# Kernel tuning notes

Hardware: AMD Instinct MI355X
Metric: run time of the kernel (lower is better)

## Reference

```python
import jax, jax.numpy as jnp
import numpy as np

N = 50000
E = 800000
HID = 256
HEADS1, C1 = 8, 32   # conv1: 2*out_dim=32 per head, 8 heads, concat -> 256
HEADS2, C2 = 1, 16   # conv2: out_dim=16, 1 head
NEG_SLOPE = 0.2


def setup_inputs() -> dict:
    key = jax.random.key(0)
    ks = jax.random.split(key, 12)
    x = jax.random.normal(ks[0], (N, HID), dtype=jnp.float32)
    edge_index = jax.random.randint(ks[1], (2, E), 0, N, dtype=jnp.int64)
    # GATConv #1 params (PyG: lin weight, att_src, att_dst, bias)
    W1 = jax.random.normal(ks[2], (HID, HEADS1 * C1), dtype=jnp.float32) / np.sqrt(HID)
    a1_src = jax.random.normal(ks[3], (HEADS1, C1), dtype=jnp.float32) * 0.1
    a1_dst = jax.random.normal(ks[4], (HEADS1, C1), dtype=jnp.float32) * 0.1
    b1 = jnp.zeros((HEADS1 * C1,), dtype=jnp.float32)
    # GATConv #2 params
    W2 = jax.random.normal(ks[5], (HEADS1 * C1, HEADS2 * C2), dtype=jnp.float32) / np.sqrt(HEADS1 * C1)
    a2_src = jax.random.normal(ks[6], (HEADS2, C2), dtype=jnp.float32) * 0.1
    a2_dst = jax.random.normal(ks[7], (HEADS2, C2), dtype=jnp.float32) * 0.1
    b2 = jnp.zeros((HEADS2 * C2,), dtype=jnp.float32)
    return {"x": x, "edge_index": edge_index, "W1": W1, "a1_src": a1_src,
            "a1_dst": a1_dst, "b1": b1, "W2": W2, "a2_src": a2_src,
            "a2_dst": a2_dst, "b2": b2}


def _gat_conv(x, src, dst, W, a_src, a_dst, b, heads, ch):
    n = x.shape[0]
    h = (x @ W).reshape(n, heads, ch)                      # [N,H,C]
    alpha_s = jnp.einsum('nhc,hc->nh', h, a_src)           # [N,H]
    alpha_d = jnp.einsum('nhc,hc->nh', h, a_dst)
    e = jax.nn.leaky_relu(alpha_s[src] + alpha_d[dst], NEG_SLOPE)  # [E,H]
    # segment softmax over edges grouped by destination node
    e_max = jax.ops.segment_max(e, dst, num_segments=n)
    ex = jnp.exp(e - e_max[dst])
    denom = jax.ops.segment_sum(ex, dst, num_segments=n)
    alpha = ex / denom[dst]                                # [E,H]
    msg = h[src] * alpha[..., None]                        # [E,H,C]
    out = jax.ops.segment_sum(msg, dst, num_segments=n)    # [N,H,C]
    return out.reshape(n, heads * ch) + b


def reference(x, edge_index, W1, a1_src, a1_dst, b1, W2, a2_src, a2_dst, b2):
    n = x.shape[0]
    # add self loops (PyG GATConv default) so every segment is non-empty
    loops = jnp.arange(n, dtype=edge_index.dtype)
    src = jnp.concatenate([edge_index[0], loops])
    dst = jnp.concatenate([edge_index[1], loops])
    # DBPnet output activation (GraphTransformer treated as precomputed x):
    x0 = jax.nn.relu(x)                                    # dropout = identity (eval)
    x1 = jax.nn.relu(_gat_conv(x0, src, dst, W1, a1_src, a1_dst, b1, HEADS1, C1))
    x2 = _gat_conv(x1, src, dst, W2, a2_src, a2_dst, b2, HEADS2, C2)
    return jax.nn.softmax(x2, axis=-1)
```

## Files before the change

kernel.cpp:

```cpp
#include <hip/hip_runtime.h>
#include <hip/hip_bf16.h>

#define HID 256
#define H1H 8
#define C1 32
#define C2 16
#define NEG 0.2f

typedef unsigned short ushort_t;
typedef unsigned int uint_t;
typedef unsigned char uchar_t;
typedef __attribute__((ext_vector_type(8))) short short8;
typedef __attribute__((ext_vector_type(4))) float f32x4;
typedef __attribute__((ext_vector_type(2))) float f32x2;

__device__ __forceinline__ float lrelu(float t){ return (t >= 0.f) ? t : NEG * t; }
__device__ __forceinline__ ushort_t f2bf(float f){
    uint_t u = __float_as_uint(f);
    u = (u + 0x7fffu + ((u >> 16) & 1u)) >> 16;
    return (ushort_t)u;
}
__device__ __forceinline__ float bf_lo(uint_t p){ return __uint_as_float(p << 16); }
__device__ __forceinline__ float bf_hi(uint_t p){ return __uint_as_float(p & 0xffff0000u); }
__device__ __forceinline__ uchar_t f2fp8(float f){
    int r = __builtin_amdgcn_cvt_pk_fp8_f32(f, f, 0, false);
    return (uchar_t)(r & 0xFF);
}

#define GLOAD_LDS16(g, l) \
    __builtin_amdgcn_global_load_lds( \
        (const __attribute__((address_space(1))) void*)(g), \
        (__attribute__((address_space(3))) void*)(l), 16, 0, 0)

__global__ __launch_bounds__(256) void prep_k(const float* __restrict__ X,
                                              ushort_t* __restrict__ Xbf, long n4,
                                              const float* __restrict__ W1,
                                              ushort_t* __restrict__ W1t,
                                              const float* __restrict__ W2,
                                              ushort_t* __restrict__ W2t,
                                              const int* __restrict__ dst,
                                              int E, int Etot, int* __restrict__ deg,
                                              int* __restrict__ slot, int cnt4)
{
    int bid = blockIdx.x;
    int tid = threadIdx.x;
    if (bid < cnt4) {
        long base = (long)bid * 1024;
        #pragma unroll
        for (int q = 0; q < 4; q++) {
            long i = base + q * 256 + tid;
            if (i < E) {
                slot[i] = atomicAdd(&deg[dst[i]], 1);
            } else if (i < Etot) {
                slot[i] = atomicAdd(&deg[i - E], 1);
            }
        }
    } else if (bid < cnt4 + 64) {
        int b = bid - cnt4;
        __shared__ ushort_t sh[32][33];
        int bx = b & 7, by = b >> 3;
        int tx = tid & 31, ty = tid >> 5;
        #pragma unroll
        for (int i = 0; i < 32; i += 8)
            sh[ty + i][tx] = f2bf(W1[(long)(bx * 32 + ty + i) * 256 + by * 32 + tx]);
        __syncthreads();
        #pragma unroll
        for (int i = 0; i < 32; i += 8)
            W1t[(long)(by * 32 + ty + i) * 256 + bx * 32 + tx] = sh[tx][ty + i];
    } else if (bid == cnt4 + 64) {
        for (int idx = tid; idx < 4096; idx += 256) {
            int k = idx >> 4, c = idx & 15;
            W2t[c * 256 + k] = f2bf(W2[idx]);
        }
    } else {
        long stride = (long)2048 * 256;
        for (long i = (long)(bid - cnt4 - 65) * 256 + tid; i < n4; i += stride) {
            float4 v = ((const float4*)X)[i];
            ushort4 o;
            o.x = f2bf(fmaxf(v.x, 0.f)); o.y = f2bf(fmaxf(v.y, 0.f));
            o.z = f2bf(fmaxf(v.z, 0.f)); o.w = f2bf(fmaxf(v.w, 0.f));
            ((ushort4*)Xbf)[i] = o;
        }
    }
}

__global__ __launch_bounds__(256) void gemm1_k(const ushort_t* __restrict__ Xbf,
                                               const ushort_t* __restrict__ W1t,
                                               const float* __restrict__ a1s_g,
                                               const float* __restrict__ a1d_g,
                                               uchar_t* __restrict__ H1f8,
                                               float* __restrict__ as1,
                                               float* __restrict__ ad1, int M)
{
    __shared__ ushort_t Abuf[64 * 64];
    __shared__ ushort_t Bbuf[128 * 64];
    int tid = threadIdx.x;
    int bm = blockIdx.y * 64, bn = blockIdx.x * 128;
    int wid = tid >> 6, lane = tid & 63;
    int wr = wid >> 1, wc = wid & 1;
    int lg = lane >> 4, lm = lane & 15;

    f32x4 acc[2][4];
    #pragma unroll
    for (int m = 0; m < 2; m++)
        #pragma unroll
        for (int n = 0; n < 4; n++) acc[m][n] = (f32x4){0.f, 0.f, 0.f, 0.f};

    int rA[2], lcA[2];
    #pragma unroll
    for (int q = 0; q < 2; q++) {
        int idx = q * 256 + tid;
        rA[q] = idx >> 3;
        lcA[q] = (idx & 7) ^ (rA[q] & 7);
    }
    int rB[4], lcB[4];
    #pragma unroll
    for (int q = 0; q < 4; q++) {
        int idx = q * 256 + tid;
        rB[q] = idx >> 3;
        lcB[q] = (idx & 7) ^ (rB[q] & 7);
    }

    for (int k0 = 0; k0 < 256; k0 += 64) {
        __syncthreads();
        #pragma unroll
        for (int q = 0; q < 2; q++) {
            const ushort_t* asrc = Xbf + (long)(bm + rA[q]) * 256 + k0 + lcA[q] * 8;
            GLOAD_LDS16(asrc, Abuf + (q * 256 + wid * 64) * 8);
        }
        #pragma unroll
        for (int q = 0; q < 4; q++) {
            const ushort_t* bsrc = W1t + (long)(bn + rB[q]) * 256 + k0 + lcB[q] * 8;
            GLOAD_LDS16(bsrc, Bbuf + (q * 256 + wid * 64) * 8);
        }
        __syncthreads();
        #pragma unroll
        for (int ks = 0; ks < 2; ks++) {
            int kg = ks * 4 + lg;
            short8 af[2], bfr[4];
            #pragma unroll
            for (int m = 0; m < 2; m++) {
                int R = wr * 32 + m * 16 + lm;
                af[m] = *(const short8*)&Abuf[(R * 8 + (kg ^ (R & 7))) * 8];
            }
            #pragma unroll
            for (int n = 0; n < 4; n++) {
                int Cc = wc * 64 + n * 16 + lm;
                bfr[n] = *(const short8*)&Bbuf[(Cc * 8 + (kg ^ (Cc & 7))) * 8];
            }
            #pragma unroll
            for (int m = 0; m < 2; m++)
                #pragma unroll
                for (int n = 0; n < 4; n++)
                    acc[m][n] = __builtin_amdgcn_mfma_f32_16x16x32_bf16(af[m], bfr[n], acc[m][n], 0, 0, 0);
        }
    }

    int h0 = ((bn >> 5) + (wc << 1));
    float as_l0 = a1s_g[h0 * 32 + lm],       as_h0 = a1s_g[h0 * 32 + 16 + lm];
    float as_l1 = a1s_g[(h0 + 1) * 32 + lm], as_h1 = a1s_g[(h0 + 1) * 32 + 16 + lm];
    float ad_l0 = a1d_g[h0 * 32 + lm],       ad_h0 = a1d_g[h0 * 32 + 16 + lm];
    float ad_l1 = a1d_g[(h0 + 1) * 32 + lm], ad_h1 = a1d_g[(h0 + 1) * 32 + 16 + lm];

    #pragma unroll
    for (int m = 0; m < 2; m++) {
        #pragma unroll
        for (int r = 0; r < 4; r++) {
            int gm = bm + wr * 32 + m * 16 + lg * 4 + r;
            float s0 = acc[m][0][r] * as_l0 + acc[m][1][r] * as_h0;
            float s1 = acc[m][2][r] * as_l1 + acc[m][3][r] * as_h1;
            float d0 = acc[m][0][r] * ad_l0 + acc[m][1][r] * ad_h0;
            float d1 = acc[m][2][r] * ad_l1 + acc[m][3][r] * ad_h1;
            #pragma unroll
            for (int off = 1; off < 16; off <<= 1) {
                s0 += __shfl_xor(s0, off);
                s1 += __shfl_xor(s1, off);
                d0 += __shfl_xor(d0, off);
                d1 += __shfl_xor(d1, off);
            }
            if (gm < M) {
                uchar_t* basep = H1f8 + (long)gm * 256 + bn + wc * 64 + lm;
                #pragma unroll
                for (int n = 0; n < 4; n++)
                    basep[n * 16] = f2fp8(acc[m][n][r]);
                if (lm == 0) {
                    float2 sv = {s0, s1}, dv = {d0, d1};
                    *(float2*)&as1[(gm << 3) + h0] = sv;
                    *(float2*)&ad1[(gm << 3) + h0] = dv;
                }
            }
        }
    }
}

__global__ __launch_bounds__(256) void scan1_k(const int* __restrict__ deg,
                                               int* __restrict__ incl,
                                               int* __restrict__ bsum, int Nn)
{
    __shared__ int sh[256];
    int t = threadIdx.x;
    int base = blockIdx.x * 1024 + t * 4;
    int v0 = (base     < Nn) ? deg[base]     : 0;
    int v1 = (base + 1 < Nn) ? deg[base + 1] : 0;
    int v2 = (base + 2 < Nn) ? deg[base + 2] : 0;
    int v3 = (base + 3 < Nn) ? deg[base + 3] : 0;
    int s0 = v0, s1 = s0 + v1, s2 = s1 + v2, s3 = s2 + v3;
    sh[t] = s3;
    __syncthreads();
    for (int off = 1; off < 256; off <<= 1) {
        int x = (t >= off) ? sh[t - off] : 0;
        __syncthreads();
        sh[t] += x;
        __syncthreads();
    }
    int prev = (t > 0) ? sh[t - 1] : 0;
    if (base     < Nn) incl[base]     = prev + s0;
    if (base + 1 < Nn) incl[base + 1] = prev + s1;
    if (base + 2 < Nn) incl[base + 2] = prev + s2;
    if (base + 3 < Nn) incl[base + 3] = prev + s3;
    if (t == 255) bsum[blockIdx.x] = sh[255];
}
__global__ void scan2_k(const int* __restrict__ bsum, int* __restrict__ bpre, int nb)
{
    int t = threadIdx.x;
    int own = (t < nb) ? bsum[t] : 0;
    int v = own;
    for (int off = 1; off < 64; off <<= 1) {
        int x = __shfl_up(v, off);
        if (t >= off) v += x;
    }
    if (t < nb) bpre[t] = v - own;
}
__global__ void scan3_k(const int* __restrict__ incl, const int* __restrict__ deg,
                        const int* __restrict__ bpre, int* __restrict__ offs,
                        int Nn, int Etot)
{
    int i = blockIdx.x * 256 + threadIdx.x;
    if (i < Nn) {
        int e = bpre[i >> 10] + incl[i] - deg[i];
        offs[i] = e;
    }
    if (i == 0) offs[Nn] = Etot;
}

__global__ __launch_bounds__(256) void scatter_k(const int* __restrict__ src,
    const int* __restrict__ dst, const int* __restrict__ slot,
    const int* __restrict__ offs, int E, int Etot, int* __restrict__ srcs)
{
    long base = (long)blockIdx.x * 1024;
    #pragma unroll
    for (int q = 0; q < 4; q++) {
        long i = base + q * 256 + threadIdx.x;
        if (i < E) {
            int d = dst[i];
            srcs[offs[d] + slot[i]] = src[i];
        } else if (i < Etot) {
            int n = (int)(i - E);
            srcs[offs[n] + slot[i]] = n;
        }
    }
}

__global__ __launch_bounds__(256) void gat1_agg_k(const uchar_t* __restrict__ H1f8,
    const float* __restrict__ as1, const float* __restrict__ ad1,
    const int* __restrict__ offs, const int* __restrict__ srcs,
    const float* __restrict__ b1, ushort_t* __restrict__ X1b, int Nn)
{
    int w = (blockIdx.x << 2) + (threadIdx.x >> 6);
    if (w >= Nn) return;
    int lane = threadIdx.x & 63;
    int he = lane & 7, el = lane >> 3;
    int myh = lane >> 3;
    int beg = offs[w], end = offs[w + 1];
    int deg = end - beg;
    float adv = ad1[(w << 3) + he];
    float4 acc = {0.f, 0.f, 0.f, 0.f};

    if (deg <= 64) {
        int sv0=0,sv1=0,sv2=0,sv3=0,sv4=0,sv5=0,sv6=0,sv7=0;
        float wv0=0,wv1=0,wv2=0,wv3=0,wv4=0,wv5=0,wv6=0,wv7=0;
        {
            int j;
            j = beg + el;      if (j < end){ sv0 = srcs[j]; wv0 = __expf(lrelu(as1[(sv0<<3)+he]+adv)); }
            j = beg + 8 + el;  if (j < end){ sv1 = srcs[j]; wv1 = __expf(lrelu(as1[(sv1<<3)+he]+adv)); }
            j = beg + 16 + el; if (j < end){ sv2 = srcs[j]; wv2 = __expf(lrelu(as1[(sv2<<3)+he]+adv)); }
            j = beg + 24 + el; if (j < end){ sv3 = srcs[j]; wv3 = __expf(lrelu(as1[(sv3<<3)+he]+adv)); }
            j = beg + 32 + el; if (j < end){ sv4 = srcs[j]; wv4 = __expf(lrelu(as1[(sv4<<3)+he]+adv)); }
            j = beg + 40 + el; if (j < end){ sv5 = srcs[j]; wv5 = __expf(lrelu(as1[(sv5<<3)+he]+adv)); }
            j = beg + 48 + el; if (j < end){ sv6 = srcs[j]; wv6 = __expf(lrelu(as1[(sv6<<3)+he]+adv)); }
            j = beg + 56 + el; if (j < end){ sv7 = srcs[j]; wv7 = __expf(lrelu(as1[(sv7<<3)+he]+adv)); }
        }
        float d = ((wv0 + wv1) + (wv2 + wv3)) + ((wv4 + wv5) + (wv6 + wv7));
        #pragma unroll
        for (int off = 8; off < 64; off <<= 1) d += __shfl_xor(d, off);
        float inv = 1.f / d;
        wv0 *= inv; wv1 *= inv; wv2 *= inv; wv3 *= inv;
        wv4 *= inv; wv5 *= inv; wv6 *= inv; wv7 *= inv;

        #define GAT1_BATCH(SV, WV, Q)                                            \
        {                                                                        \
            int ne = deg - (Q << 3);                                             \
            if (ne > 0) {                                                        \
                ne = min(ne, 8);                                                 \
                int sb[8]; float wb[8];                                          \
                _Pragma("unroll")                                                \
                for (int e8 = 0; e8 < 8; e8++) {                                 \
                    sb[e8] = __shfl(SV, e8 << 3);                                \
                    wb[e8] = __shfl(WV, (e8 << 3) + myh);                        \
                }                                                                \
                if (ne == 8) {                                                   \
                    _Pragma("unroll")                                            \
                    for (int e8 = 0; e8 < 8; e8++) {                             \
                        uint_t v = ((const uint_t*)(H1f8 + ((long)sb[e8] << 8)))[lane]; \
                        f32x2 lo = __builtin_amdgcn_cvt_pk_f32_fp8((int)v, false); \
                        f32x2 hi = __builtin_amdgcn_cvt_pk_f32_fp8((int)v, true);  \
                        acc.x += wb[e8] * lo[0];                                 \
                        acc.y += wb[e8] * lo[1];                                 \
                        acc.z += wb[e8] * hi[0];                                 \
                        acc.w += wb[e8] * hi[1];                                 \
                    }                                                            \
                } else {                                                         \
                    _Pragma("unroll")                                            \
                    for (int e8 = 0; e8 < 8; e8++) {                             \
                        if (e8 < ne) {                                           \
                            uint_t v = ((const uint_t*)(H1f8 + ((long)sb[e8] << 8)))[lane]; \
                            f32x2 lo = __builtin_amdgcn_cvt_pk_f32_fp8((int)v, false); \
                            f32x2 hi = __builtin_amdgcn_cvt_pk_f32_fp8((int)v, true);  \
                            acc.x += wb[e8] * lo[0];                             \
                            acc.y += wb[e8] * lo[1];                             \
                            acc.z += wb[e8] * hi[0];                             \
                            acc.w += wb[e8] * hi[1];                             \
                        }                                                        \
                    }                                                            \
                }                                                                \
            }                                                                    \
        }
        GAT1_BATCH(sv0, wv0, 0)
        GAT1_BATCH(sv1, wv1, 1)
        GAT1_BATCH(sv2, wv2, 2)
        GAT1_BATCH(sv3, wv3, 3)
        GAT1_BATCH(sv4, wv4, 4)
        GAT1_BATCH(sv5, wv5, 5)
        GAT1_BATCH(sv6, wv6, 6)
        GAT1_BATCH(sv7, wv7, 7)
        #undef GAT1_BATCH
    } else {
        float dA = 0.f, dB = 0.f;
        for (int j0 = beg; j0 < end; j0 += 16) {
            int j = j0 + el, jb = j0 + 8 + el;
            if (j < end)  dA += __expf(lrelu(as1[(srcs[j] << 3) + he] + adv));
            if (jb < end) dB += __expf(lrelu(as1[(srcs[jb] << 3) + he] + adv));
        }
        float d = dA + dB;
        #pragma unroll
        for (int off = 8; off < 64; off <<= 1) d += __shfl_xor(d, off);
        float inv = 1.f / d;
        for (int j0 = beg; j0 < end; j0 += 8) {
            int j = j0 + el;
            int s = 0; float wv = 0.f;
            if (j < end) {
                s = srcs[j];
                wv = __expf(lrelu(as1[(s << 3) + he] + adv)) * inv;
            }
            int ne = min(end - j0, 8);
            int sb[8]; float wb[8];
            #pragma unroll
            for (int e8 = 0; e8 < 8; e8++) {
                sb[e8] = __shfl(s, e8 << 3);
                wb[e8] = __shfl(wv, (e8 << 3) + myh);
            }
            #pragma unroll
            for (int e8 = 0; e8 < 8; e8++) {
                if (e8 < ne) {
                    uint_t v = ((const uint_t*)(H1f8 + ((long)sb[e8] << 8)))[lane];
                    f32x2 lo = __builtin_amdgcn_cvt_pk_f32_fp8((int)v, false);
                    f32x2 hi = __builtin_amdgcn_cvt_pk_f32_fp8((int)v, true);
                    acc.x += wb[e8] * lo[0];
                    acc.y += wb[e8] * lo[1];
                    acc.z += wb[e8] * hi[0];
                    acc.w += wb[e8] * hi[1];
                }
            }
        }
    }

    float4 bb = ((const float4*)b1)[lane];
    float o0 = fmaxf(acc.x + bb.x, 0.f);
    float o1 = fmaxf(acc.y + bb.y, 0.f);
    float o2 = fmaxf(acc.z + bb.z, 0.f);
    float o3 = fmaxf(acc.w + bb.w, 0.f);
    uint2 ov;
    ov.x = (uint_t)f2bf(o0) | ((uint_t)f2bf(o1) << 16);
    ov.y = (uint_t)f2bf(o2) | ((uint_t)f2bf(o3) << 16);
    ((uint2*)(X1b + ((long)w << 8)))[lane] = ov;
}

__global__ __launch_bounds__(256) void gemm2_k(const ushort_t* __restrict__ X1b,
    const ushort_t* __restrict__ W2t, const float* __restrict__ a2s_w,
    const float* __restrict__ a2d_w, float* __restrict__ H2,
    float* __restrict__ as2, float* __restrict__ ad2, int Nn)
{
    int wid = threadIdx.x >> 6, lane = threadIdx.x & 63;
    int row0 = blockIdx.x * 64 + wid * 16;
    if (row0 >= Nn) return;
    int lm = lane & 15, lg = lane >> 4;
    f32x4 acc = (f32x4){0.f, 0.f, 0.f, 0.f};
    const ushort_t* arow = X1b + (long)(row0 + lm) * 256 + lg * 8;
    const ushort_t* brow = W2t + lm * 256 + lg * 8;
    #pragma unroll
    for (int k0 = 0; k0 < 256; k0 += 32) {
        short8 af = *(const short8*)(arow + k0);
        short8 bf = *(const short8*)(brow + k0);
        acc = __builtin_amdgcn_mfma_f32_16x16x32_bf16(af, bf, acc, 0, 0, 0);
    }
    float a2sv = a2s_w[lm], a2dv = a2d_w[lm];
    #pragma unroll
    for (int r = 0; r < 4; r++) {
        int grow = row0 + lg * 4 + r;
        if (grow < Nn) H2[(grow << 4) + lm] = acc[r];
        float s = acc[r] * a2sv, d2 = acc[r] * a2dv;
        #pragma unroll
        for (int off = 1; off < 16; off <<= 1) {
            s += __shfl_xor(s, off);
            d2 += __shfl_xor(d2, off);
        }
        if (lm == 0 && grow < Nn) { as2[grow] = s; ad2[grow] = d2; }
    }
}

__global__ __launch_bounds__(256) void gat2_agg_k(const float* __restrict__ H2,
    const float* __restrict__ as2, const float* __restrict__ ad2,
    const int* __restrict__ offs, const int* __restrict__ srcs,
    const float* __restrict__ b2, float* __restrict__ out, int Nn)
{
    int w = (blockIdx.x << 2) + (threadIdx.x >> 6);
    if (w >= Nn) return;
    int lane = threadIdx.x & 63;
    int beg = offs[w], end = offs[w + 1];
    int deg = end - beg;
    float adv = ad2[w];
    int c = lane & 15, eg = lane >> 4;
    float acc = 0.f;

    if (deg <= 64) {
        int j = beg + lane;
        int s_l = 0; float w_l = 0.f;
        if (j < end) { s_l = srcs[j]; w_l = __expf(lrelu(as2[s_l] + adv)); }
        float d = w_l;
        #pragma unroll
        for (int off = 1; off < 64; off <<= 1) d += __shfl_xor(d, off);
        float w_n = w_l / d;
        for (int j0 = 0; j0 < deg; j0 += 4) {
            int jj = j0 + eg;
            int s = __shfl(s_l, jj);
            float wv = __shfl(w_n, jj);
            if (jj < deg)
                acc += wv * H2[(s << 4) + c];
        }
    } else {
        float d = 0.f;
        for (int j = beg + lane; j < end; j += 64)
            d += __expf(lrelu(as2[srcs[j]] + adv));
        #pragma unroll
        for (int off = 1; off < 64; off <<= 1) d += __shfl_xor(d, off);
        float inv = 1.f / d;
        for (int j0 = beg; j0 < end; j0 += 4) {
            int j = j0 + eg;
            if (j < end) {
                int s = srcs[j];
                float wv = __expf(lrelu(as2[s] + adv)) * inv;
                acc += wv * H2[(s << 4) + c];
            }
        }
    }
    acc += __shfl_xor(acc, 16);
    acc += __shfl_xor(acc, 32);
    float v = acc + b2[c];
    float mx = v;
    #pragma unroll
    for (int off = 1; off < 16; off <<= 1) mx = fmaxf(mx, __shfl_xor(mx, off));
    float ex = __expf(v - mx);
    float se = ex;
    #pragma unroll
    for (int off = 1; off < 16; off <<= 1) se += __shfl_xor(se, off);
    if (eg == 0) out[(w << 4) + c] = ex / se;
}

extern "C" void kernel_launch(void* const* d_in, const int* in_sizes, int n_in,
                              void* d_out, int out_size, void* d_ws, size_t ws_size,
                              hipStream_t stream)
{
    const float* x    = (const float*)d_in[0];
    const int*   ei   = (const int*)d_in[1];
    const float* W1   = (const float*)d_in[2];
    const float* a1s  = (const float*)d_in[3];
    const float* a1d  = (const float*)d_in[4];
    const float* b1   = (const float*)d_in[5];
    const float* W2   = (const float*)d_in[6];
    const float* a2s  = (const float*)d_in[7];
    const float* a2d  = (const float*)d_in[8];
    const float* b2   = (const float*)d_in[9];
    float* out = (float*)d_out;

    int N = in_sizes[0] / HID;
    int E = in_sizes[1] / 2;
    int Etot = E + N;
    const int* src = ei;
    const int* dst = ei + E;

    char* p = (char*)d_ws;
    auto alloc = [&](size_t bytes) {
        void* r = (void*)p;
        p += (bytes + 255) & ~(size_t)255;
        return r;
    };
    ushort_t* xbf  = (ushort_t*)alloc((size_t)N * 256 * 2);
    uchar_t*  h1f8 = (uchar_t*)alloc((size_t)N * 256);
    ushort_t* x1b  = (ushort_t*)alloc((size_t)N * 256 * 2);
    ushort_t* w1t  = (ushort_t*)alloc((size_t)256 * 256 * 2);
    ushort_t* w2t  = (ushort_t*)alloc((size_t)16 * 256 * 2);
    float* h2      = (float*)alloc((size_t)N * 16 * 4);
    float* as1     = (float*)alloc((size_t)N * 8 * 4);
    float* ad1     = (float*)alloc((size_t)N * 8 * 4);
    float* as2v    = (float*)alloc((size_t)N * 4);
    float* ad2v    = (float*)alloc((size_t)N * 4);
    int*   deg     = (int*)alloc((size_t)N * 4);
    int*   incl    = (int*)alloc((size_t)N * 4);
    int*   offs    = (int*)alloc((size_t)(N + 1) * 4);
    int*   bsum    = (int*)alloc(256 * 4);
    int*   bpre    = (int*)alloc(256 * 4);
    int*   srcs    = (int*)alloc((size_t)Etot * 4);
    int*   slot    = (int*)alloc((size_t)Etot * 4);

    int nb = (N + 1023) / 1024;
    int cnt4 = (Etot + 1023) / 1024;
    int scat_blocks = (Etot + 1023) / 1024;

    hipMemsetAsync(deg, 0, (size_t)N * 4, stream);
    hipLaunchKernelGGL(prep_k, dim3(cnt4 + 65 + 2048), dim3(256), 0, stream,
                       x, xbf, (long)N * 64, W1, w1t, W2, w2t, dst, E, Etot,
                       deg, slot, cnt4);
    hipLaunchKernelGGL(scan1_k, dim3(nb), dim3(256), 0, stream, deg, incl, bsum, N);
    hipLaunchKernelGGL(scan2_k, dim3(1), dim3(64), 0, stream, bsum, bpre, nb);
    hipLaunchKernelGGL(scan3_k, dim3((N + 255) / 256), dim3(256), 0, stream,
                       incl, deg, bpre, offs, N, Etot);
    hipLaunchKernelGGL(scatter_k, dim3(scat_blocks), dim3(256), 0, stream,
                       src, dst, slot, offs, E, Etot, srcs);
    dim3 g1(2, (N + 63) / 64);
    hipLaunchKernelGGL(gemm1_k, g1, dim3(256), 0, stream,
                       xbf, w1t, a1s, a1d, h1f8, as1, ad1, N);
    hipLaunchKernelGGL(gat1_agg_k, dim3((N + 3) / 4), dim3(256), 0, stream,
                       h1f8, as1, ad1, offs, srcs, b1, x1b, N);
    hipLaunchKernelGGL(gemm2_k, dim3((N + 63) / 64), dim3(256), 0, stream,
                       x1b, w2t, a2s, a2d, h2, as2v, ad2v, N);
    hipLaunchKernelGGL(gat2_agg_k, dim3((N + 3) / 4), dim3(256), 0, stream,
                       h2, as2v, ad2v, offs, srcs, b2, out, N);
}
```

Measured before the change: 189.9 us.

## Move degree counting into GEMM1 launch and place self-loops analytically

The atomic degree-count and slot assignment for real edges moves out of the prep kernel and into extra blocks of the first GEMM launch. This lets the atomics overlap with the matrix multiply, and the GEMM now runs before the scan and scatter stages. Self-loops no longer use atomics: the scan adds one to each degree and the scatter writes each self-loop into the last slot of its segment. The cost is a longer dependency chain in front of the scan and a changed edge order inside each segment, which can alter floating-point summation order.

```diff
diff --git a/kernel.cpp b/kernel.cpp
--- a/kernel.cpp
+++ b/kernel.cpp
@@ -37,28 +37,13 @@
                                               const float* __restrict__ W1,
                                               ushort_t* __restrict__ W1t,
                                               const float* __restrict__ W2,
-                                              ushort_t* __restrict__ W2t,
-                                              const int* __restrict__ dst,
-                                              int E, int Etot, int* __restrict__ deg,
-                                              int* __restrict__ slot, int cnt4)
+                                              ushort_t* __restrict__ W2t)
 {
     int bid = blockIdx.x;
     int tid = threadIdx.x;
-    if (bid < cnt4) {
-        long base = (long)bid * 1024;
-        #pragma unroll
-        for (int q = 0; q < 4; q++) {
-            long i = base + q * 256 + tid;
-            if (i < E) {
-                slot[i] = atomicAdd(&deg[dst[i]], 1);
-            } else if (i < Etot) {
-                slot[i] = atomicAdd(&deg[i - E], 1);
-            }
-        }
-    } else if (bid < cnt4 + 64) {
-        int b = bid - cnt4;
+    if (bid < 64) {
         __shared__ ushort_t sh[32][33];
-        int bx = b & 7, by = b >> 3;
+        int bx = bid & 7, by = bid >> 3;
         int tx = tid & 31, ty = tid >> 5;
         #pragma unroll
         for (int i = 0; i < 32; i += 8)
@@ -67,14 +52,14 @@
         #pragma unroll
         for (int i = 0; i < 32; i += 8)
             W1t[(long)(by * 32 + ty + i) * 256 + bx * 32 + tx] = sh[tx][ty + i];
-    } else if (bid == cnt4 + 64) {
+    } else if (bid == 64) {
         for (int idx = tid; idx < 4096; idx += 256) {
             int k = idx >> 4, c = idx & 15;
             W2t[c * 256 + k] = f2bf(W2[idx]);
         }
     } else {
         long stride = (long)2048 * 256;
-        for (long i = (long)(bid - cnt4 - 65) * 256 + tid; i < n4; i += stride) {
+        for (long i = (long)(bid - 65) * 256 + tid; i < n4; i += stride) {
             float4 v = ((const float4*)X)[i];
             ushort4 o;
             o.x = f2bf(fmaxf(v.x, 0.f)); o.y = f2bf(fmaxf(v.y, 0.f));
@@ -90,12 +75,28 @@
                                                const float* __restrict__ a1d_g,
                                                uchar_t* __restrict__ H1f8,
                                                float* __restrict__ as1,
-                                               float* __restrict__ ad1, int M)
+                                               float* __restrict__ ad1, int M,
+                                               const int* __restrict__ dst, int E,
+                                               int* __restrict__ deg,
+                                               int* __restrict__ slot, int cntB)
 {
     __shared__ ushort_t Abuf[64 * 64];
     __shared__ ushort_t Bbuf[128 * 64];
+    int bid = blockIdx.x;
     int tid = threadIdx.x;
-    int bm = blockIdx.y * 64, bn = blockIdx.x * 128;
+
+    if (bid < cntB) {
+        long base = (long)bid * 1024;
+        #pragma unroll
+        for (int q = 0; q < 4; q++) {
+            long i = base + q * 256 + tid;
+            if (i < E) slot[i] = atomicAdd(&deg[dst[i]], 1);
+        }
+        return;
+    }
+
+    int bid2 = bid - cntB;
+    int bm = (bid2 >> 1) * 64, bn = (bid2 & 1) * 128;
     int wid = tid >> 6, lane = tid & 63;
     int wr = wid >> 1, wc = wid & 1;
     int lg = lane >> 4, lm = lane & 15;
@@ -200,10 +201,10 @@
     __shared__ int sh[256];
     int t = threadIdx.x;
     int base = blockIdx.x * 1024 + t * 4;
-    int v0 = (base     < Nn) ? deg[base]     : 0;
-    int v1 = (base + 1 < Nn) ? deg[base + 1] : 0;
-    int v2 = (base + 2 < Nn) ? deg[base + 2] : 0;
-    int v3 = (base + 3 < Nn) ? deg[base + 3] : 0;
+    int v0 = (base     < Nn) ? deg[base]     + 1 : 0;
+    int v1 = (base + 1 < Nn) ? deg[base + 1] + 1 : 0;
+    int v2 = (base + 2 < Nn) ? deg[base + 2] + 1 : 0;
+    int v3 = (base + 3 < Nn) ? deg[base + 3] + 1 : 0;
     int s0 = v0, s1 = s0 + v1, s2 = s1 + v2, s3 = s2 + v3;
     sh[t] = s3;
     __syncthreads();
@@ -237,7 +238,7 @@
 {
     int i = blockIdx.x * 256 + threadIdx.x;
     if (i < Nn) {
-        int e = bpre[i >> 10] + incl[i] - deg[i];
+        int e = bpre[i >> 10] + incl[i] - (deg[i] + 1);
         offs[i] = e;
     }
     if (i == 0) offs[Nn] = Etot;
@@ -256,7 +257,7 @@
             srcs[offs[d] + slot[i]] = src[i];
         } else if (i < Etot) {
             int n = (int)(i - E);
-            srcs[offs[n] + slot[i]] = n;
+            srcs[offs[n + 1] - 1] = n;
         }
     }
 }
@@ -533,22 +534,22 @@
     int*   slot    = (int*)alloc((size_t)Etot * 4);
 
     int nb = (N + 1023) / 1024;
-    int cnt4 = (Etot + 1023) / 1024;
+    int cntB = (E + 1023) / 1024;
     int scat_blocks = (Etot + 1023) / 1024;
+    int gemmB = 2 * ((N + 63) / 64);
 
     hipMemsetAsync(deg, 0, (size_t)N * 4, stream);
-    hipLaunchKernelGGL(prep_k, dim3(cnt4 + 65 + 2048), dim3(256), 0, stream,
-                       x, xbf, (long)N * 64, W1, w1t, W2, w2t, dst, E, Etot,
-                       deg, slot, cnt4);
+    hipLaunchKernelGGL(prep_k, dim3(65 + 2048), dim3(256), 0, stream,
+                       x, xbf, (long)N * 64, W1, w1t, W2, w2t);
+    hipLaunchKernelGGL(gemm1_k, dim3(cntB + gemmB), dim3(256), 0, stream,
+                       xbf, w1t, a1s, a1d, h1f8, as1, ad1, N,
+                       dst, E, deg, slot, cntB);
     hipLaunchKernelGGL(scan1_k, dim3(nb), dim3(256), 0, stream, deg, incl, bsum, N);
     hipLaunchKernelGGL(scan2_k, dim3(1), dim3(64), 0, stream, bsum, bpre, nb);
     hipLaunchKernelGGL(scan3_k, dim3((N + 255) / 256), dim3(256), 0, stream,
                        incl, deg, bpre, offs, N, Etot);
     hipLaunchKernelGGL(scatter_k, dim3(scat_blocks), dim3(256), 0, stream,
                        src, dst, slot, offs, E, Etot, srcs);
-    dim3 g1(2, (N + 63) / 64);
-    hipLaunchKernelGGL(gemm1_k, g1, dim3(256), 0, stream,
-                       xbf, w1t, a1s, a1d, h1f8, as1, ad1, N);
     hipLaunchKernelGGL(gat1_agg_k, dim3((N + 3) / 4), dim3(256), 0, stream,
                        h1f8, as1, ad1, offs, srcs, b1, x1b, N);
     hipLaunchKernelGGL(gemm2_k, dim3((N + 63) / 64), dim3(256), 0, stream,
```

Result: no change. 189.9 us (-0.0%).
